# Optimization experiments

Hardware: AMD Instinct MI355X
Metric: run time of the kernel (lower is better)

## Reference

```python
import jax, jax.numpy as jnp
import numpy as np

B, N, D, H = 2, 2048, 768, 12
HD = D // H  # 64


def apply_rotary_embed(x, thetas):
    # x: (..., N, HD), thetas: (N, HD) broadcast over leading dims
    x1, x2 = jnp.split(x, 2, axis=-1)
    x_rot = jnp.concatenate([-x2, x1], axis=-1)
    return x * jnp.cos(thetas) + x_rot * jnp.sin(thetas)


def setup_inputs() -> dict:
    key = jax.random.key(0)
    ks = jax.random.split(key, 5)
    s = 0.02
    return {
        "x": jax.random.normal(ks[0], (B, N, D), dtype=jnp.float32),
        "pos_embed": jax.random.normal(ks[1], (N, HD), dtype=jnp.float32),
        "Wqkv": jax.random.normal(ks[2], (3 * D, D), dtype=jnp.float32) * s,
        "Wproj": jax.random.normal(ks[3], (D, D), dtype=jnp.float32) * s,
        "bproj": jnp.zeros((D,), dtype=jnp.float32),
    }


def reference(x, pos_embed, Wqkv, Wproj, bproj):
    Bb, Nn, Dd = x.shape
    # fused QKV projection (torch Linear: x @ W.T), no bias
    qkv = jnp.einsum('bnd,ed->bne', x, Wqkv)                 # (B, N, 3D)
    qkv = qkv.reshape(Bb, Nn, 3, H, HD).transpose(2, 0, 3, 1, 4)  # (3, B, H, N, HD)
    q, k, v = qkv[0], qkv[1], qkv[2]
    # rotary embedding on q and k
    q = apply_rotary_embed(q, pos_embed)
    k = apply_rotary_embed(k, pos_embed)
    # scaled dot-product attention (non-causal, no mask, no dropout)
    scale = 1.0 / jnp.sqrt(jnp.asarray(HD, dtype=x.dtype))
    scores = jnp.einsum('bhqd,bhkd->bhqk', q, k) * scale     # (B, H, N, N)
    attn = jax.nn.softmax(scores, axis=-1)
    out = jnp.einsum('bhqk,bhkd->bhqd', attn, v)             # (B, H, N, HD)
    out = out.transpose(0, 2, 1, 3).reshape(Bb, Nn, Dd)      # (B, N, D)
    # output projection (with bias)
    return jnp.einsum('bnd,ed->bne', out, Wproj) + bproj
```

## Files before the change

### kernel.cpp

```cpp
#include <hip/hip_runtime.h>
#include <stdint.h>

typedef __attribute__((ext_vector_type(8))) short short8;
typedef __attribute__((ext_vector_type(4))) float floatx4;
typedef __attribute__((ext_vector_type(16))) float floatx16;

#define BB 2
#define NN 2048
#define DD 768
#define HH 12
#define HDD 64
#define MM (BB*NN)

__device__ __forceinline__ unsigned short f2bf(float f) {
  unsigned int u = __builtin_bit_cast(unsigned int, f);
  u += 0x7fffu + ((u >> 16) & 1u);
  return (unsigned short)(u >> 16);
}
__device__ __forceinline__ float bf2f(unsigned short u) {
  unsigned int v = ((unsigned int)u) << 16;
  return __builtin_bit_cast(float, v);
}

__device__ __forceinline__ void gld16(const unsigned short* g, unsigned short* l) {
  __builtin_amdgcn_global_load_lds(
      (const __attribute__((address_space(1))) void*)g,
      (__attribute__((address_space(3))) void*)l, 16, 0, 0);
}

__global__ void cvt_all(const float* __restrict__ x, const float* __restrict__ wq,
                        const float* __restrict__ wp, unsigned short* __restrict__ xb,
                        unsigned short* __restrict__ wqb, unsigned short* __restrict__ wpb) {
  const int n1 = MM*DD/4, n2 = 3*DD*DD/4, n3 = DD*DD/4;
  int i = blockIdx.x * blockDim.x + threadIdx.x;
  const float* s; unsigned short* d; int j;
  if (i < n1)            { s = x;  d = xb;  j = i; }
  else if (i < n1+n2)    { s = wq; d = wqb; j = i - n1; }
  else if (i < n1+n2+n3) { s = wp; d = wpb; j = i - n1 - n2; }
  else return;
  float4 v = reinterpret_cast<const float4*>(s)[j];
  unsigned int lo = (unsigned int)f2bf(v.x) | ((unsigned int)f2bf(v.y) << 16);
  unsigned int hi = (unsigned int)f2bf(v.z) | ((unsigned int)f2bf(v.w) << 16);
  reinterpret_cast<uint2*>(d)[j] = make_uint2(lo, hi);
}

template<int MODE, int MT>
__global__ __launch_bounds__(256) void gemm_bt(
    const unsigned short* __restrict__ A,
    const unsigned short* __restrict__ Bt,
    void* __restrict__ Cout, const float* __restrict__ bias,
    int Nn, int K)
{
  constexpr int MTC = MT / 32;
  __shared__ __align__(16) unsigned short as_[MT*32];
  __shared__ __align__(16) unsigned short bs_[128*32];
  const int t = threadIdx.x;
  const int w = t >> 6, lane = t & 63;
  const int quad = lane >> 4, l16 = lane & 15;
  const int wm = (w >> 1) * (MT/2), wn = (w & 1) * 64;
  const int m0 = blockIdx.y * MT, n0 = blockIdx.x * 128;

  const floatx4 fz = {0.f, 0.f, 0.f, 0.f};
  floatx4 acc[MTC][4];
#pragma unroll
  for (int mt = 0; mt < MTC; mt++)
#pragma unroll
    for (int nt = 0; nt < 4; nt++) acc[mt][nt] = fz;

  for (int k0 = 0; k0 < K; k0 += 32) {
    __syncthreads();
#pragma unroll
    for (int i = 0; i < MT/64; i++) {
      int c = t + i * 256;
      gld16(&A[(size_t)(m0 + (c >> 2))*K + k0 + (c & 3)*8], &as_[c*8]);
    }
#pragma unroll
    for (int i = 0; i < 2; i++) {
      int c = t + i * 256;
      gld16(&Bt[(size_t)(n0 + (c >> 2))*K + k0 + (c & 3)*8], &bs_[c*8]);
    }
    __syncthreads();
    short8 af[MTC], bfr[4];
#pragma unroll
    for (int mt = 0; mt < MTC; mt++)
      af[mt] = *reinterpret_cast<const short8*>(&as_[(wm + mt*16 + l16)*32 + quad*8]);
#pragma unroll
    for (int nt = 0; nt < 4; nt++)
      bfr[nt] = *reinterpret_cast<const short8*>(&bs_[(wn + nt*16 + l16)*32 + quad*8]);
#pragma unroll
    for (int mt = 0; mt < MTC; mt++)
#pragma unroll
      for (int nt = 0; nt < 4; nt++)
        acc[mt][nt] = __builtin_amdgcn_mfma_f32_16x16x32_bf16(af[mt], bfr[nt], acc[mt][nt], 0, 0, 0);
  }
#pragma unroll
  for (int mt = 0; mt < MTC; mt++)
#pragma unroll
    for (int nt = 0; nt < 4; nt++)
#pragma unroll
      for (int r = 0; r < 4; r++) {
        int gm = m0 + wm + mt*16 + quad*4 + r;
        int gn = n0 + wn + nt*16 + l16;
        float v = acc[mt][nt][r];
        if (MODE == 0)
          reinterpret_cast<unsigned short*>(Cout)[(size_t)gm * Nn + gn] = f2bf(v);
        else
          reinterpret_cast<float*>(Cout)[(size_t)gm * Nn + gn] = v + bias[gn];
      }
}

__global__ __launch_bounds__(256) void rope_relayout(
    const unsigned short* __restrict__ qkv, const float* __restrict__ pos,
    unsigned short* __restrict__ qb, unsigned short* __restrict__ kb,
    unsigned short* __restrict__ vb)
{
  __shared__ __align__(16) unsigned short vt_l[64*72];
  const int n0 = blockIdx.x * 64;
  const int bh = blockIdx.y;
  const int b = bh / HH, hh = bh % HH;
  const int t = threadIdx.x;
  const int nl = t >> 2, j = t & 3;
  const int n = n0 + nl;
  const size_t qrow = (size_t)(b*NN + n) * (3*DD) + hh*HDD;

  union U8 { int4 v; unsigned short u[8]; };
  U8 qlo, qhi, klo, khi, vlo, vhi, qolo, qohi, kolo, kohi;
  qlo.v = *(const int4*)&qkv[qrow + j*8];
  qhi.v = *(const int4*)&qkv[qrow + 32 + j*8];
  klo.v = *(const int4*)&qkv[qrow + DD + j*8];
  khi.v = *(const int4*)&qkv[qrow + DD + 32 + j*8];
  vlo.v = *(const int4*)&qkv[qrow + 2*DD + j*8];
  vhi.v = *(const int4*)&qkv[qrow + 2*DD + 32 + j*8];
  float4 tl0 = *(const float4*)&pos[n*HDD + j*8];
  float4 tl1 = *(const float4*)&pos[n*HDD + j*8 + 4];
  float4 th0 = *(const float4*)&pos[n*HDD + 32 + j*8];
  float4 th1 = *(const float4*)&pos[n*HDD + 32 + j*8 + 4];
  float tl[8] = {tl0.x,tl0.y,tl0.z,tl0.w,tl1.x,tl1.y,tl1.z,tl1.w};
  float th[8] = {th0.x,th0.y,th0.z,th0.w,th1.x,th1.y,th1.z,th1.w};
#pragma unroll
  for (int e = 0; e < 8; e++) {
    float sl, cl, sh, ch;
    __sincosf(tl[e], &sl, &cl);
    __sincosf(th[e], &sh, &ch);
    float q1 = bf2f(qlo.u[e]), q2 = bf2f(qhi.u[e]);
    float k1 = bf2f(klo.u[e]), k2 = bf2f(khi.u[e]);
    qolo.u[e] = f2bf((q1*cl - q2*sl) * 0.125f);
    qohi.u[e] = f2bf((q2*ch + q1*sh) * 0.125f);
    kolo.u[e] = f2bf(k1*cl - k2*sl);
    kohi.u[e] = f2bf(k2*ch + k1*sh);
  }
  size_t obase = ((size_t)bh*NN + n) * HDD;
  *(int4*)&qb[obase + j*8] = qolo.v;
  *(int4*)&qb[obase + 32 + j*8] = qohi.v;
  *(int4*)&kb[obase + ((j       ^ (n & 7)) * 8)] = kolo.v;
  *(int4*)&kb[obase + (((j + 4) ^ (n & 7)) * 8)] = kohi.v;
#pragma unroll
  for (int e = 0; e < 8; e++) {
    vt_l[(j*8 + e)*72 + nl]      = vlo.u[e];
    vt_l[(j*8 + 32 + e)*72 + nl] = vhi.u[e];
  }
  __syncthreads();
  int hd = t >> 2;
#pragma unroll
  for (int u = 0; u < 2; u++) {
    int cc = (t & 3) + u * 4;
    int4 vv = *(const int4*)&vt_l[hd*72 + cc*8];
    int cg = ((n0 & 64) >> 3) + cc;
    int cswz = cg ^ (hd & 7);
    *(int4*)&vb[((size_t)bh*HDD + hd)*NN + (size_t)(n0 & ~127) + cswz*8] = vv;
  }
}

__global__ __launch_bounds__(256) void flash_attn(
    const unsigned short* __restrict__ qb, const unsigned short* __restrict__ kb,
    const unsigned short* __restrict__ vb, unsigned short* __restrict__ ob)
{
  __shared__ __align__(16) unsigned short ks[128*64];
  __shared__ __align__(16) unsigned short vt[64*128];
  __shared__ __align__(16) unsigned short ps[64*128];
  __shared__ __align__(16) float lsd[128];
  const int qt = blockIdx.x, bh = blockIdx.y;
  const int b = bh / HH, hh = bh % HH;
  const int t = threadIdx.x;
  const int w = t >> 6, lane = t & 63;
  const int l32 = lane & 31, hf = lane >> 5;
  const int gq = w >> 1;
  const int kh = w & 1;
  const int q0 = qt * 64;
  const size_t kbase = (size_t)bh * (NN*HDD);

  short8 qf[4];
  {
    const unsigned short* qp = &qb[((size_t)bh*NN + q0 + gq*32 + l32)*HDD + hf*8];
#pragma unroll
    for (int s = 0; s < 4; s++) qf[s] = *(const short8*)&qp[s*16];
  }
  floatx16 fz16;
#pragma unroll
  for (int z = 0; z < 16; z++) fz16[z] = 0.f;
  floatx16 oacc[2];
  oacc[0] = fz16; oacc[1] = fz16;
  float lrow = 0.f;

  for (int kt = 0; kt < NN/128; kt++) {
    __syncthreads();
#pragma unroll
    for (int i = 0; i < 4; i++) {
      int c = i*256 + t;
      gld16(&kb[kbase + (size_t)kt*8192 + c*8], &ks[c*8]);
      gld16(&vb[kbase + (size_t)(c >> 4)*NN + kt*128 + (c & 15)*8], &vt[c*8]);
    }
    __syncthreads();

    floatx16 sv[2];
#pragma unroll
    for (int tt = 0; tt < 2; tt++) {
      floatx16 acc;
#pragma unroll
      for (int z = 0; z < 16; z++) acc[z] = 0.f;
      int t2 = kh*2 + tt;
      int row = t2*32 + l32;
#pragma unroll
      for (int s = 0; s < 4; s++) {
        int cd = (2*s + hf) ^ (l32 & 7);
        short8 kf = *(const short8*)&ks[row*64 + cd*8];
        acc = __builtin_amdgcn_mfma_f32_32x32x16_bf16(kf, qf[s], acc, 0, 0, 0);
      }
      sv[tt] = acc;
    }
    float rs = 0.f;
    unsigned short* pr = &ps[(gq*32 + l32)*128];
#pragma unroll
    for (int tt = 0; tt < 2; tt++) {
      int t2 = kh*2 + tt;
      float pv_[16];
#pragma unroll
      for (int r = 0; r < 16; r++) { pv_[r] = __expf(sv[tt][r]); rs += pv_[r]; }
#pragma unroll
      for (int g = 0; g < 4; g++) {
        unsigned int x0 = __builtin_bit_cast(unsigned int, pv_[4*g+0]);
        unsigned int x1 = __builtin_bit_cast(unsigned int, pv_[4*g+1]);
        unsigned int x2 = __builtin_bit_cast(unsigned int, pv_[4*g+2]);
        unsigned int x3 = __builtin_bit_cast(unsigned int, pv_[4*g+3]);
        unsigned int lo = __builtin_amdgcn_perm(x1, x0, 0x07060302u);
        unsigned int hi = __builtin_amdgcn_perm(x3, x2, 0x07060302u);
        int slot = (t2*4 + g) ^ (l32 & 7);
        *(uint2*)&pr[slot*8 + hf*4] = make_uint2(lo, hi);
      }
    }
    rs += __shfl_xor(rs, 32);
    lrow += rs;
#pragma unroll
    for (int ss = 0; ss < 4; ss++) {
      int s2 = kh*4 + ss;
      int ca = (s2*2 + hf) ^ (l32 & 7);
      short8 pf = *(const short8*)&pr[ca*8];
#pragma unroll
      for (int ht = 0; ht < 2; ht++) {
        int hd = ht*32 + l32;
        short8 vf = *(const short8*)&vt[hd*128 + ca*8];
        oacc[ht] = __builtin_amdgcn_mfma_f32_32x32x16_bf16(pf, vf, oacc[ht], 0, 0, 0);
      }
    }
  }
  __syncthreads();
  float* om = (float*)ps;
  if (kh) {
    float* base = om + gq*2048;
#pragma unroll
    for (int ht = 0; ht < 2; ht++)
#pragma unroll
      for (int g = 0; g < 4; g++)
#pragma unroll
        for (int e = 0; e < 4; e++) {
          int ql = hf*4 + g*8 + e;
          base[ql*64 + ht*32 + l32] = oacc[ht][4*g+e];
        }
  }
  if (hf == 0) lsd[w*32 + l32] = lrow;
  __syncthreads();
  if (!kh) {
    float* base = om + gq*2048;
#pragma unroll
    for (int g = 0; g < 4; g++)
#pragma unroll
      for (int e = 0; e < 4; e++) {
        int ql = hf*4 + g*8 + e;
        float l = lsd[gq*64 + ql] + lsd[gq*64 + 32 + ql];
        float inv = 1.f / l;
        int qrow = q0 + gq*32 + ql;
#pragma unroll
        for (int ht = 0; ht < 2; ht++) {
          float v = oacc[ht][4*g+e] + base[ql*64 + ht*32 + l32];
          ob[((size_t)(b*NN + qrow))*DD + hh*HDD + ht*32 + l32] = f2bf(v * inv);
        }
      }
  }
}

extern "C" void kernel_launch(void* const* d_in, const int* in_sizes, int n_in,
                              void* d_out, int out_size, void* d_ws, size_t ws_size,
                              hipStream_t stream)
{
  const float* x     = (const float*)d_in[0];
  const float* pos   = (const float*)d_in[1];
  const float* Wqkv  = (const float*)d_in[2];
  const float* Wproj = (const float*)d_in[3];
  const float* bproj = (const float*)d_in[4];

  unsigned short* p = (unsigned short*)d_ws;
  unsigned short* xb     = p; p += (size_t)MM*DD;
  unsigned short* wqkvb  = p; p += (size_t)3*DD*DD;
  unsigned short* wprojb = p; p += (size_t)DD*DD;
  unsigned short* qkvrm  = p; p += (size_t)MM*3*DD;
  unsigned short* qb     = p; p += (size_t)BB*HH*NN*HDD;
  unsigned short* kb     = p; p += (size_t)BB*HH*NN*HDD;
  unsigned short* vb     = p; p += (size_t)BB*HH*NN*HDD;
  unsigned short* ob     = qkvrm;

  const int ncvt = MM*DD/4 + 3*DD*DD/4 + DD*DD/4;
  cvt_all<<<ncvt/256, 256, 0, stream>>>(x, Wqkv, Wproj, xb, wqkvb, wprojb);

  gemm_bt<0,64><<<dim3(3*DD/128, MM/64), 256, 0, stream>>>(xb, wqkvb, qkvrm, nullptr, 3*DD, DD);
  rope_relayout<<<dim3(NN/64, BB*HH), 256, 0, stream>>>(qkvrm, pos, qb, kb, vb);
  flash_attn<<<dim3(NN/64, BB*HH), 256, 0, stream>>>(qb, kb, vb, ob);
  gemm_bt<1,64><<<dim3(DD/128, MM/64), 256, 0, stream>>>(ob, wprojb, (float*)d_out, bproj, DD, DD);
}
```

Before: 175.5 us.

## Fuse rotary embedding and Q/K/V relayout into QKV GEMM epilogue

The separate rope_relayout kernel is removed. The QKV projection GEMM epilogue now applies the rotary embedding and scale to Q and K and writes them straight into the per-head swizzled layouts that flash attention expects. V is written transposed with packed stores. This avoids writing and re-reading the intermediate row-major qkv buffer and saves one kernel launch. In exchange the epilogue uses scattered 2-byte stores for Q/K and recomputes sincos per GEMM tile.

Measured after the change: 172.4 us. No clear change (-1.8%).

```diff
diff --git a/kernel.cpp b/kernel.cpp
--- a/kernel.cpp
+++ b/kernel.cpp
@@ -49,7 +49,10 @@
     const unsigned short* __restrict__ A,
     const unsigned short* __restrict__ Bt,
     void* __restrict__ Cout, const float* __restrict__ bias,
-    int Nn, int K)
+    int Nn, int K,
+    const float* __restrict__ pos,
+    unsigned short* __restrict__ qb2, unsigned short* __restrict__ kb2,
+    unsigned short* __restrict__ vb2)
 {
   constexpr int MTC = MT / 32;
   __shared__ __align__(16) unsigned short as_[MT*32];
@@ -93,81 +96,67 @@
       for (int nt = 0; nt < 4; nt++)
         acc[mt][nt] = __builtin_amdgcn_mfma_f32_16x16x32_bf16(af[mt], bfr[nt], acc[mt][nt], 0, 0, 0);
   }
-#pragma unroll
-  for (int mt = 0; mt < MTC; mt++)
-#pragma unroll
-    for (int nt = 0; nt < 4; nt++)
-#pragma unroll
-      for (int r = 0; r < 4; r++) {
-        int gm = m0 + wm + mt*16 + quad*4 + r;
-        int gn = n0 + wn + nt*16 + l16;
-        float v = acc[mt][nt][r];
-        if (MODE == 0)
-          reinterpret_cast<unsigned short*>(Cout)[(size_t)gm * Nn + gn] = f2bf(v);
-        else
-          reinterpret_cast<float*>(Cout)[(size_t)gm * Nn + gn] = v + bias[gn];
-      }
-}
-
-__global__ __launch_bounds__(256) void rope_relayout(
-    const unsigned short* __restrict__ qkv, const float* __restrict__ pos,
-    unsigned short* __restrict__ qb, unsigned short* __restrict__ kb,
-    unsigned short* __restrict__ vb)
-{
-  __shared__ __align__(16) unsigned short vt_l[64*72];
-  const int n0 = blockIdx.x * 64;
-  const int bh = blockIdx.y;
-  const int b = bh / HH, hh = bh % HH;
-  const int t = threadIdx.x;
-  const int nl = t >> 2, j = t & 3;
-  const int n = n0 + nl;
-  const size_t qrow = (size_t)(b*NN + n) * (3*DD) + hh*HDD;
-
-  union U8 { int4 v; unsigned short u[8]; };
-  U8 qlo, qhi, klo, khi, vlo, vhi, qolo, qohi, kolo, kohi;
-  qlo.v = *(const int4*)&qkv[qrow + j*8];
-  qhi.v = *(const int4*)&qkv[qrow + 32 + j*8];
-  klo.v = *(const int4*)&qkv[qrow + DD + j*8];
-  khi.v = *(const int4*)&qkv[qrow + DD + 32 + j*8];
-  vlo.v = *(const int4*)&qkv[qrow + 2*DD + j*8];
-  vhi.v = *(const int4*)&qkv[qrow + 2*DD + 32 + j*8];
-  float4 tl0 = *(const float4*)&pos[n*HDD + j*8];
-  float4 tl1 = *(const float4*)&pos[n*HDD + j*8 + 4];
-  float4 th0 = *(const float4*)&pos[n*HDD + 32 + j*8];
-  float4 th1 = *(const float4*)&pos[n*HDD + 32 + j*8 + 4];
-  float tl[8] = {tl0.x,tl0.y,tl0.z,tl0.w,tl1.x,tl1.y,tl1.z,tl1.w};
-  float th[8] = {th0.x,th0.y,th0.z,th0.w,th1.x,th1.y,th1.z,th1.w};
-#pragma unroll
-  for (int e = 0; e < 8; e++) {
-    float sl, cl, sh, ch;
-    __sincosf(tl[e], &sl, &cl);
-    __sincosf(th[e], &sh, &ch);
-    float q1 = bf2f(qlo.u[e]), q2 = bf2f(qhi.u[e]);
-    float k1 = bf2f(klo.u[e]), k2 = bf2f(khi.u[e]);
-    qolo.u[e] = f2bf((q1*cl - q2*sl) * 0.125f);
-    qohi.u[e] = f2bf((q2*ch + q1*sh) * 0.125f);
-    kolo.u[e] = f2bf(k1*cl - k2*sl);
-    kohi.u[e] = f2bf(k2*ch + k1*sh);
-  }
-  size_t obase = ((size_t)bh*NN + n) * HDD;
-  *(int4*)&qb[obase + j*8] = qolo.v;
-  *(int4*)&qb[obase + 32 + j*8] = qohi.v;
-  *(int4*)&kb[obase + ((j       ^ (n & 7)) * 8)] = kolo.v;
-  *(int4*)&kb[obase + (((j + 4) ^ (n & 7)) * 8)] = kohi.v;
-#pragma unroll
-  for (int e = 0; e < 8; e++) {
-    vt_l[(j*8 + e)*72 + nl]      = vlo.u[e];
-    vt_l[(j*8 + 32 + e)*72 + nl] = vhi.u[e];
-  }
-  __syncthreads();
-  int hd = t >> 2;
-#pragma unroll
-  for (int u = 0; u < 2; u++) {
-    int cc = (t & 3) + u * 4;
-    int4 vv = *(const int4*)&vt_l[hd*72 + cc*8];
-    int cg = ((n0 & 64) >> 3) + cc;
-    int cswz = cg ^ (hd & 7);
-    *(int4*)&vb[((size_t)bh*HDD + hd)*NN + (size_t)(n0 & ~127) + cswz*8] = vv;
+  if (MODE == 2) {
+    const int region = n0 / DD;
+    const int nl0 = n0 - region * DD;
+    const int head = (nl0 + wn) / HDD;
+    if (region < 2) {
+#pragma unroll
+      for (int mt = 0; mt < MTC; mt++)
+#pragma unroll
+        for (int r = 0; r < 4; r++) {
+          int gm = m0 + wm + mt*16 + quad*4 + r;
+          int bq = gm >> 11, nseq = gm & (NN-1);
+          size_t base = ((size_t)(bq*HH + head)*NN + nseq) * HDD;
+#pragma unroll
+          for (int nt = 0; nt < 2; nt++) {
+            int hd = nt*16 + l16;
+            float t1 = pos[nseq*HDD + hd], t2 = pos[nseq*HDD + hd + 32];
+            float s1, c1, s2, c2;
+            __sincosf(t1, &s1, &c1);
+            __sincosf(t2, &s2, &c2);
+            float a1 = acc[mt][nt][r], a2 = acc[mt][nt+2][r];
+            if (region == 0) {
+              qb2[base + hd]      = f2bf((a1*c1 - a2*s1) * 0.125f);
+              qb2[base + hd + 32] = f2bf((a2*c2 + a1*s2) * 0.125f);
+            } else {
+              int sl1 = (hd >> 3) ^ (nseq & 7);
+              int sl2 = ((hd >> 3) + 4) ^ (nseq & 7);
+              kb2[base + sl1*8 + (hd & 7)] = f2bf(a1*c1 - a2*s1);
+              kb2[base + sl2*8 + (hd & 7)] = f2bf(a2*c2 + a1*s2);
+            }
+          }
+        }
+    } else {
+#pragma unroll
+      for (int mt = 0; mt < MTC; mt++)
+#pragma unroll
+        for (int nt = 0; nt < 4; nt++) {
+          int hd = nt*16 + l16;
+          int seqb = m0 + wm + mt*16 + quad*4;
+          int bq = seqb >> 11, nsb = seqb & (NN-1);
+          unsigned int p0 = (unsigned int)f2bf(acc[mt][nt][0]) | ((unsigned int)f2bf(acc[mt][nt][1]) << 16);
+          unsigned int p1 = (unsigned int)f2bf(acc[mt][nt][2]) | ((unsigned int)f2bf(acc[mt][nt][3]) << 16);
+          int slot = ((nsb >> 3) & 15) ^ (hd & 7);
+          size_t addr = ((size_t)(bq*HH + head)*HDD + hd) * NN + (nsb & ~127) + slot*8 + (nsb & 7);
+          *(uint2*)&vb2[addr] = make_uint2(p0, p1);
+        }
+    }
+  } else {
+#pragma unroll
+    for (int mt = 0; mt < MTC; mt++)
+#pragma unroll
+      for (int nt = 0; nt < 4; nt++)
+#pragma unroll
+        for (int r = 0; r < 4; r++) {
+          int gm = m0 + wm + mt*16 + quad*4 + r;
+          int gn = n0 + wn + nt*16 + l16;
+          float v = acc[mt][nt][r];
+          if (MODE == 0)
+            reinterpret_cast<unsigned short*>(Cout)[(size_t)gm * Nn + gn] = f2bf(v);
+          else
+            reinterpret_cast<float*>(Cout)[(size_t)gm * Nn + gn] = v + bias[gn];
+        }
   }
 }
 
@@ -312,17 +301,17 @@
   unsigned short* xb     = p; p += (size_t)MM*DD;
   unsigned short* wqkvb  = p; p += (size_t)3*DD*DD;
   unsigned short* wprojb = p; p += (size_t)DD*DD;
-  unsigned short* qkvrm  = p; p += (size_t)MM*3*DD;
+  unsigned short* ob     = p; p += (size_t)MM*DD;
   unsigned short* qb     = p; p += (size_t)BB*HH*NN*HDD;
   unsigned short* kb     = p; p += (size_t)BB*HH*NN*HDD;
   unsigned short* vb     = p; p += (size_t)BB*HH*NN*HDD;
-  unsigned short* ob     = qkvrm;
 
   const int ncvt = MM*DD/4 + 3*DD*DD/4 + DD*DD/4;
   cvt_all<<<ncvt/256, 256, 0, stream>>>(x, Wqkv, Wproj, xb, wqkvb, wprojb);
 
-  gemm_bt<0,64><<<dim3(3*DD/128, MM/64), 256, 0, stream>>>(xb, wqkvb, qkvrm, nullptr, 3*DD, DD);
-  rope_relayout<<<dim3(NN/64, BB*HH), 256, 0, stream>>>(qkvrm, pos, qb, kb, vb);
+  gemm_bt<2,64><<<dim3(3*DD/128, MM/64), 256, 0, stream>>>(
+      xb, wqkvb, nullptr, nullptr, 3*DD, DD, pos, qb, kb, vb);
   flash_attn<<<dim3(NN/64, BB*HH), 256, 0, stream>>>(qb, kb, vb, ob);
-  gemm_bt<1,64><<<dim3(DD/128, MM/64), 256, 0, stream>>>(ob, wprojb, (float*)d_out, bproj, DD, DD);
-}
+  gemm_bt<1,64><<<dim3(DD/128, MM/64), 256, 0, stream>>>(
+      ob, wprojb, (float*)d_out, bproj, DD, DD, nullptr, nullptr, nullptr, nullptr);
+}
```
